# Optimization experiments

Measured on AMD Instinct MI355X. Metric: run time of the kernel, lower is better.

Reference implementation:

```python
import jax, jax.numpy as jnp
import numpy as np

KH = KW = 3
K = KH * KW
OG = 1  # offset_groups
WG = 1  # weight_groups
DIL = 1

def _conv_same(x, w):
    # stride-1 SAME NCHW conv, matching the keras offset/mask convs
    return jax.lax.conv_general_dilated(
        x, w, window_strides=(1, 1), padding='SAME',
        dimension_numbers=('NCHW', 'OIHW', 'NCHW'))

def _deform_conv2d(x, w, offset, mask):
    # x: [B,C,H,W]; w: [F, C//WG, KH, KW]
    # offset: [B, OG*2*K, H, W] laid out as (og, k, {dy,dx});
    # mask:   [B, OG*K, H, W]
    B, C, H, W = x.shape
    F = w.shape[0]
    pad_h = ((KH - 1) * DIL) // 2
    pad_w = ((KW - 1) * DIL) // 2
    ky = jnp.arange(KH) * DIL - pad_h
    kx = jnp.arange(KW) * DIL - pad_w
    kyy, kxx = jnp.meshgrid(ky, kx, indexing='ij')
    kyy = kyy.reshape(K).astype(x.dtype)
    kxx = kxx.reshape(K).astype(x.dtype)

    off = offset.reshape(B, OG, K, 2, H, W)
    dy = off[:, :, :, 0]  # [B,OG,K,H,W]
    dx = off[:, :, :, 1]
    oy = jnp.arange(H, dtype=x.dtype)
    ox = jnp.arange(W, dtype=x.dtype)
    y = oy[None, None, None, :, None] + kyy[None, None, :, None, None] + dy
    xq = ox[None, None, None, None, :] + kxx[None, None, :, None, None] + dx

    y0 = jnp.floor(y)
    x0 = jnp.floor(xq)
    wy = y - y0   # [B,OG,K,H,W]
    wx = xq - x0
    y0i = y0.astype(jnp.int32)
    x0i = x0.astype(jnp.int32)

    Cg = C // OG
    xg = x.reshape(B, OG, Cg, H * W)

    def gather(yi, xi):
        valid = (yi >= 0) & (yi < H) & (xi >= 0) & (xi < W)
        idx = jnp.clip(yi, 0, H - 1) * W + jnp.clip(xi, 0, W - 1)
        flat = idx.reshape(B, OG, 1, K * H * W)
        v = jnp.take_along_axis(xg, flat, axis=3)   # [B,OG,Cg,K*H*W]
        v = v.reshape(B, OG, Cg, K, H, W)
        return v * valid[:, :, None].astype(x.dtype)

    v00 = gather(y0i, x0i)
    v01 = gather(y0i, x0i + 1)
    v10 = gather(y0i + 1, x0i)
    v11 = gather(y0i + 1, x0i + 1)
    wy_ = wy[:, :, None]
    wx_ = wx[:, :, None]
    samp = (v00 * (1 - wy_) * (1 - wx_) + v01 * (1 - wy_) * wx_
            + v10 * wy_ * (1 - wx_) + v11 * wy_ * wx_)  # [B,OG,Cg,K,H,W]
    m = mask.reshape(B, OG, K, H, W)[:, :, None]
    samp = samp * m
    wr = w.reshape(F, OG, Cg, K)
    return jnp.einsum('bgckhw,fgck->bfhw', samp, wr)


def setup_inputs() -> dict:
    key = jax.random.key(0)
    k1, k2, k3, k4 = jax.random.split(key, 4)
    B, C, H, W = 8, 256, 64, 64
    F = 256
    x = jax.random.normal(k1, (B, C, H, W), dtype=jnp.float32)
    w_offset = jax.random.normal(k2, (OG * 2 * K, C, KH, KW), dtype=jnp.float32) * 0.01
    w_mask = jax.random.normal(k3, (OG * K, C, KH, KW), dtype=jnp.float32) * 0.01
    w_deform = jax.random.normal(k4, (F, C // WG, KH, KW), dtype=jnp.float32) * 0.05
    return {'x': x, 'w_offset': w_offset, 'w_mask': w_mask, 'w_deform': w_deform}


def reference(x, w_offset, w_mask, w_deform):
    offset = _conv_same(x, w_offset)                 # [B, 2K, H, W]
    mask = jax.nn.sigmoid(_conv_same(x, w_mask))     # [B, K, H, W]
    return _deform_conv2d(x, w_deform, offset, mask)
```

## Files before the change

### kernel.cpp

```cpp
#include <hip/hip_runtime.h>
#include <hip/hip_bf16.h>
#include <hip/hip_fp16.h>
#include <math.h>

constexpr int Bn = 8, Cn = 256, Hn = 64, Wn = 64, Fn = 256, Kn = 9;
constexpr int HWn = Hn * Wn;
constexpr int NM = Bn * Kn * HWn;
constexpr int NCH = 4;

using frag_ab = __attribute__((ext_vector_type(8))) short;
using frag_h  = __attribute__((ext_vector_type(8))) _Float16;
using f32x4   = __attribute__((ext_vector_type(4))) float;

__device__ inline ushort f2bf(float f) {
    union { float f; uint32_t u; } un{f};
    return (ushort)((un.u + 0x7FFF + ((un.u >> 16) & 1)) >> 16);
}
__device__ inline ushort f2h(float f) {
    __half h = __float2half_rn(f);
    return *reinterpret_cast<ushort*>(&h);
}

__global__ __launch_bounds__(256) void wtrans2(const float* __restrict__ wd,
                                               ushort* __restrict__ wB) {
    int i = blockIdx.x * 256 + threadIdx.x;
    if (i >= Fn * Cn * Kn) return;
    int ci = i & 7, fi = (i >> 3) & 15, G = (i >> 7) & 31, ft = (i >> 12) & 15, k = i >> 16;
    int f = ft * 16 + fi, c = G * 8 + ci;
    wB[i] = f2h(wd[(f * Cn + c) * 9 + k]);
}

__global__ __launch_bounds__(256) void wpack27(const float* __restrict__ wo,
                                               const float* __restrict__ wm,
                                               ushort* __restrict__ wA) {
    int i = blockIdx.x * 256 + threadIdx.x;
    if (i >= 73728) return;
    int ci = i & 7, l = (i >> 3) & 63, mt = (i >> 9) & 1, cblk = (i >> 10) & 7, tap = i >> 13;
    int m = mt * 16 + (l & 15);
    int c = cblk * 32 + ((l >> 4) & 3) * 8 + ci;
    float v = 0.f;
    if (m < 18)      v = wo[(m * Cn + c) * 9 + tap];
    else if (m < 27) v = wm[((m - 18) * Cn + c) * 9 + tap];
    wA[i] = f2bf(v);
}

__global__ __launch_bounds__(256) void xpose(const float* __restrict__ x,
                                             __half2* __restrict__ xh) {
    int i = blockIdx.x * 256 + threadIdx.x;
    int p = i & 4095, q = (i >> 12) & 3, b = i >> 14;
    const float* xp = x + (size_t)b * Cn * HWn + p;
    __half2* op = xh + (((size_t)b * 4096 + p) << 7) + q * 32;
#pragma unroll
    for (int j = 0; j < 32; ++j) {
        int c = q * 64 + 2 * j;
        op[j] = __float22half2_rn(make_float2(xp[(size_t)c * HWn],
                                              xp[(size_t)(c + 1) * HWn]));
    }
}

__global__ __launch_bounds__(256) void offconv27(const float* __restrict__ x,
                                                 const ushort* __restrict__ wA,
                                                 float* __restrict__ part) {
    __shared__ ushort xs[4][66][40];
    const int t = threadIdx.x;
    const int l = t & 63, w = t >> 6;
    const int li = l & 15, lg = l >> 4;
    const int rb = blockIdx.x, ch = blockIdx.y, b = blockIdx.z;
    const int h0 = rb * 2;
    const int rw = w >> 1, pt0 = (w & 1) * 2;

    f32x4 acc[2][2];
#pragma unroll
    for (int mt = 0; mt < 2; ++mt)
#pragma unroll
        for (int q = 0; q < 2; ++q) acc[mt][q] = (f32x4)0.f;

    const float* xb = x + (size_t)b * Cn * HWn;

#pragma unroll 1
    for (int cc = 0; cc < 2; ++cc) {
        const int cbase = ch * 64 + cc * 32;
        __syncthreads();
        for (int j = t; j < 1056; j += 256) {
            int cq = j / 264;
            int rem = j - cq * 264;
            int r = rem / 66, col = rem - r * 66;
            int rg = h0 - 1 + r, cg = col - 1;
            ushort u[8];
            if ((unsigned)rg < (unsigned)Hn && (unsigned)cg < (unsigned)Wn) {
                const float* xp = xb + (size_t)(cbase + cq * 8) * HWn + (rg << 6) + cg;
#pragma unroll
                for (int jj = 0; jj < 8; ++jj) u[jj] = f2bf(xp[(size_t)jj * HWn]);
            } else {
#pragma unroll
                for (int jj = 0; jj < 8; ++jj) u[jj] = 0;
            }
            *(int4*)&xs[r][col][cq * 8] =
                make_int4(u[0] | (u[1] << 16), u[2] | (u[3] << 16),
                          u[4] | (u[5] << 16), u[6] | (u[7] << 16));
        }
        __syncthreads();
        const int cblk = ch * 2 + cc;
#pragma unroll
        for (int tap = 0; tap < 9; ++tap) {
            const int ky = tap / 3, kx = tap - 3 * (tap / 3);
            frag_ab a0 = *(const frag_ab*)(wA + (size_t)((tap * 8 + cblk) * 2) * 512 + l * 8);
            frag_ab a1 = *(const frag_ab*)(wA + (size_t)((tap * 8 + cblk) * 2 + 1) * 512 + l * 8);
#pragma unroll
            for (int q = 0; q < 2; ++q) {
                frag_ab bf = *(const frag_ab*)&xs[rw + ky][(pt0 + q) * 16 + li + kx][lg * 8];
                acc[0][q] = __builtin_amdgcn_mfma_f32_16x16x32_bf16(a0, bf, acc[0][q], 0, 0, 0);
                acc[1][q] = __builtin_amdgcn_mfma_f32_16x16x32_bf16(a1, bf, acc[1][q], 0, 0, 0);
            }
        }
    }

    const int h = h0 + rw;
#pragma unroll
    for (int mt = 0; mt < 2; ++mt)
#pragma unroll
        for (int j = 0; j < 4; ++j) {
            int m = mt * 16 + lg * 4 + j;
            if (m < 27) {
#pragma unroll
                for (int q = 0; q < 2; ++q) {
                    int pixel = (pt0 + q) * 16 + li;
                    part[((size_t)((ch * Bn + b) * 27 + m) << 12) + (h << 6) + pixel] =
                        acc[mt][q][j];
                }
            }
        }
}

__global__ __launch_bounds__(256) void metafin9(const float* __restrict__ part,
                                                int4* __restrict__ mpack) {
    const int k = blockIdx.y;
    const int idx = blockIdx.x * 256 + threadIdx.x;
    const int b = idx >> 12, p = idx & 4095;
    const int h = p >> 6, w = p & 63;

    float dy = 0.f, dx = 0.f, ms = 0.f;
#pragma unroll
    for (int ch = 0; ch < NCH; ++ch) {
        size_t base = ((size_t)((ch * Bn + b) * 27) << 12) + p;
        dy += part[base + ((size_t)(2 * k) << 12)];
        dx += part[base + ((size_t)(2 * k + 1) << 12)];
        ms += part[base + ((size_t)(18 + k) << 12)];
    }
    float m = 1.f / (1.f + expf(-ms));
    float yy = (float)(h + k / 3 - 1) + dy;
    float xx = (float)(w + k % 3 - 1) + dx;
    float y0f = floorf(yy), x0f = floorf(xx);
    float wy = yy - y0f, wx = xx - x0f;
    int y0 = (int)y0f, x0 = (int)x0f;
    int y1 = y0 + 1, x1 = x0 + 1;
    bool vy0 = (unsigned)y0 < (unsigned)Hn;
    bool vx0 = (unsigned)x0 < (unsigned)Wn;
    bool vy1 = (unsigned)y1 < (unsigned)Hn;
    bool vx1 = (unsigned)x1 < (unsigned)Wn;
    int cy0 = min(max(y0, 0), Hn - 1), cx0 = min(max(x0, 0), Wn - 1);
    int cy1 = min(max(y1, 0), Hn - 1), cx1 = min(max(x1, 0), Wn - 1);
    float w00 = (vy0 && vx0) ? (1.f - wy) * (1.f - wx) * m : 0.f;
    float w01 = (vy0 && vx1) ? (1.f - wy) * wx * m : 0.f;
    float w10 = (vy1 && vx0) ? wy * (1.f - wx) * m : 0.f;
    float w11 = (vy1 && vx1) ? wy * wx * m : 0.f;
    int i00 = (cy0 << 6) + cx0, i01 = (cy0 << 6) + cx1;
    int i10 = (cy1 << 6) + cx0, i11 = (cy1 << 6) + cx1;
    union { struct { __half a, bh; } h; int i; } pz, pw;
    pz.h.a = __float2half_rn(w00); pz.h.bh = __float2half_rn(w01);
    pw.h.a = __float2half_rn(w10); pw.h.bh = __float2half_rn(w11);
    int q = ((b * 9 + k) << 12) + p;
    mpack[q] = make_int4(i00 | (i01 << 16), i10 | (i11 << 16), pz.i, pw.i);
}

__global__ __launch_bounds__(512, 4) void dconv(const uint32_t* __restrict__ xh,
                                                const ushort* __restrict__ wB,
                                                const int4* __restrict__ mpack,
                                                float* __restrict__ out) {
    __shared__ ushort sl[2][64][64];
    __shared__ int4 ml[9][64];
    const int t = threadIdx.x;
    const int l = t & 63, w = t >> 6;
    const int li = l & 15, lg = l >> 4;
    const int pu = (w << 3) + (l >> 3);
    const int g  = l & 7;
    const int b = blockIdx.x;
    const int p0 = blockIdx.y << 6;

    f32x4 acc[2][4];
#pragma unroll
    for (int a = 0; a < 2; ++a)
#pragma unroll
        for (int q = 0; q < 4; ++q) acc[a][q] = (f32x4)0.f;

    const uint32_t* xb = xh + ((size_t)b << 19);

    for (int j = t; j < 576; j += 512)
        ml[j >> 6][j & 63] = mpack[((b * 9 + (j >> 6)) << 12) + p0 + (j & 63)];
    __syncthreads();

    auto STAGE = [&](int s, int buf) {
        const int k = s % 9, ch = s / 9;
        const int4 m = ml[k][pu];
        const int i00 = m.x & 0xFFFF, i01 = ((unsigned)m.x) >> 16;
        const int i10 = m.y & 0xFFFF, i11 = ((unsigned)m.y) >> 16;
        union { int i; __half2 h; } uz, uw;
        uz.i = m.z; uw.i = m.w;
        const uint32_t* base = xb + (ch << 5) + (g << 2);
        uint4 v00 = *(const uint4*)(base + (size_t)i00 * 128);
        uint4 v01 = *(const uint4*)(base + (size_t)i01 * 128);
        uint4 v10 = *(const uint4*)(base + (size_t)i10 * 128);
        uint4 v11 = *(const uint4*)(base + (size_t)i11 * 128);
        const __half2 w00 = __half2half2(__low2half(uz.h));
        const __half2 w01 = __half2half2(__high2half(uz.h));
        const __half2 w10 = __half2half2(__low2half(uw.h));
        const __half2 w11 = __half2half2(__high2half(uw.h));
        uint4 rr;
        {
            __half2 r = __hmul2(w00, *(__half2*)&v00.x);
            r = __hfma2(w01, *(__half2*)&v01.x, r);
            r = __hfma2(w10, *(__half2*)&v10.x, r);
            r = __hfma2(w11, *(__half2*)&v11.x, r);
            rr.x = *(uint32_t*)&r;
        }
        {
            __half2 r = __hmul2(w00, *(__half2*)&v00.y);
            r = __hfma2(w01, *(__half2*)&v01.y, r);
            r = __hfma2(w10, *(__half2*)&v10.y, r);
            r = __hfma2(w11, *(__half2*)&v11.y, r);
            rr.y = *(uint32_t*)&r;
        }
        {
            __half2 r = __hmul2(w00, *(__half2*)&v00.z);
            r = __hfma2(w01, *(__half2*)&v01.z, r);
            r = __hfma2(w10, *(__half2*)&v10.z, r);
            r = __hfma2(w11, *(__half2*)&v11.z, r);
            rr.z = *(uint32_t*)&r;
        }
        {
            __half2 r = __hmul2(w00, *(__half2*)&v00.w);
            r = __hfma2(w01, *(__half2*)&v01.w, r);
            r = __hfma2(w10, *(__half2*)&v10.w, r);
            r = __hfma2(w11, *(__half2*)&v11.w, r);
            rr.w = *(uint32_t*)&r;
        }
        *(uint4*)&sl[buf][pu][(g ^ (pu & 7)) << 3] = rr;
    };

    auto COMPUTE = [&](int s, int buf) {
        const int k = s % 9, ch = s / 9;
        const ushort* wp = wB + ((size_t)((k * 16 + 2 * w) * 512 + ch * 128)) * 8;
#pragma unroll
        for (int h = 0; h < 2; ++h) {
            frag_h bq[4];
#pragma unroll
            for (int pt = 0; pt < 4; ++pt)
                bq[pt] = *(const frag_h*)&sl[buf][pt * 16 + li]
                                           [((((h << 2) | lg) ^ (l & 7)) << 3)];
#pragma unroll
            for (int ft = 0; ft < 2; ++ft) {
                frag_h a = *(const frag_h*)(wp + (size_t)(ft * 512 + h * 64 + l) * 8);
#pragma unroll
                for (int pt = 0; pt < 4; ++pt)
                    acc[ft][pt] = __builtin_amdgcn_mfma_f32_16x16x32_f16(
                        a, bq[pt], acc[ft][pt], 0, 0, 0);
            }
        }
    };

    STAGE(0, 0);
    __syncthreads();
#pragma unroll 1
    for (int s = 0; s < 36; ++s) {
        const int cur = s & 1;
        if (s + 1 < 36) STAGE(s + 1, cur ^ 1);
        COMPUTE(s, cur);
        __syncthreads();
    }

    float* ob = out + (size_t)b * Fn * HWn + p0;
#pragma unroll
    for (int ft = 0; ft < 2; ++ft)
#pragma unroll
        for (int j = 0; j < 4; ++j) {
            int f = w * 32 + ft * 16 + lg * 4 + j;
#pragma unroll
            for (int pt = 0; pt < 4; ++pt)
                ob[(size_t)f * HWn + pt * 16 + li] = acc[ft][pt][j];
        }
}

extern "C" void kernel_launch(void* const* d_in, const int* in_sizes, int n_in,
                              void* d_out, int out_size, void* d_ws, size_t ws_size,
                              hipStream_t stream) {
    const float* x  = (const float*)d_in[0];
    const float* wo = (const float*)d_in[1];
    const float* wm = (const float*)d_in[2];
    const float* wd = (const float*)d_in[3];
    float* out = (float*)d_out;

    int4*     mpack = (int4*)d_ws;
    char*     region = (char*)d_ws + (size_t)NM * 16;
    float*    part  = (float*)region;
    ushort*   wBp   = (ushort*)region;
    __half2*  xhh   = (__half2*)(region + 1179648);
    uint32_t* xhu   = (uint32_t*)(region + 1179648);
    ushort*   wA27  = (ushort*)(region + 18874368);

    wpack27<<<dim3(288), dim3(256), 0, stream>>>(wo, wm, wA27);
    offconv27<<<dim3(32, NCH, Bn), dim3(256), 0, stream>>>(x, wA27, part);
    metafin9<<<dim3(Bn * HWn / 256, 9), dim3(256), 0, stream>>>(part, mpack);
    wtrans2<<<dim3((Fn * Cn * Kn + 255) / 256), dim3(256), 0, stream>>>(wd, wBp);
    xpose<<<dim3(Bn * 4 * HWn / 256), dim3(256), 0, stream>>>(x, xhh);
    dconv<<<dim3(Bn, HWn / 64), dim3(512), 0, stream>>>(xhu, wBp, mpack, out);
}
```

Measured before the change: 106.1 us.

## Split gather into register prefetch and finish stages for deeper pipelining

Splits the bilinear gather stage into a global-load step that fills registers and a finish step that blends and writes to LDS. Loads for step s+2 are issued before the MFMA compute of step s, so gather latency is hidden across two compute phases instead of one. The main loop is unrolled by two with alternating register sets. This costs extra VGPRs for two in-flight sets of 4 uint4 loads, which may reduce occupancy.

```diff
diff --git a/kernel.cpp b/kernel.cpp
--- a/kernel.cpp
+++ b/kernel.cpp
@@ -199,49 +199,56 @@
         ml[j >> 6][j & 63] = mpack[((b * 9 + (j >> 6)) << 12) + p0 + (j & 63)];
     __syncthreads();
 
-    auto STAGE = [&](int s, int buf) {
+    struct GR { uint4 c00, c01, c10, c11; int wz, ww; };
+    GR gA, gB;
+
+    auto LOADG = [&](int s, GR& gr) {
         const int k = s % 9, ch = s / 9;
         const int4 m = ml[k][pu];
         const int i00 = m.x & 0xFFFF, i01 = ((unsigned)m.x) >> 16;
         const int i10 = m.y & 0xFFFF, i11 = ((unsigned)m.y) >> 16;
+        const uint32_t* base = xb + (ch << 5) + (g << 2);
+        gr.c00 = *(const uint4*)(base + (size_t)i00 * 128);
+        gr.c01 = *(const uint4*)(base + (size_t)i01 * 128);
+        gr.c10 = *(const uint4*)(base + (size_t)i10 * 128);
+        gr.c11 = *(const uint4*)(base + (size_t)i11 * 128);
+        gr.wz = m.z; gr.ww = m.w;
+    };
+
+    auto FINISH = [&](const GR& gr, int buf) {
         union { int i; __half2 h; } uz, uw;
-        uz.i = m.z; uw.i = m.w;
-        const uint32_t* base = xb + (ch << 5) + (g << 2);
-        uint4 v00 = *(const uint4*)(base + (size_t)i00 * 128);
-        uint4 v01 = *(const uint4*)(base + (size_t)i01 * 128);
-        uint4 v10 = *(const uint4*)(base + (size_t)i10 * 128);
-        uint4 v11 = *(const uint4*)(base + (size_t)i11 * 128);
+        uz.i = gr.wz; uw.i = gr.ww;
         const __half2 w00 = __half2half2(__low2half(uz.h));
         const __half2 w01 = __half2half2(__high2half(uz.h));
         const __half2 w10 = __half2half2(__low2half(uw.h));
         const __half2 w11 = __half2half2(__high2half(uw.h));
         uint4 rr;
         {
-            __half2 r = __hmul2(w00, *(__half2*)&v00.x);
-            r = __hfma2(w01, *(__half2*)&v01.x, r);
-            r = __hfma2(w10, *(__half2*)&v10.x, r);
-            r = __hfma2(w11, *(__half2*)&v11.x, r);
+            __half2 r = __hmul2(w00, *(const __half2*)&gr.c00.x);
+            r = __hfma2(w01, *(const __half2*)&gr.c01.x, r);
+            r = __hfma2(w10, *(const __half2*)&gr.c10.x, r);
+            r = __hfma2(w11, *(const __half2*)&gr.c11.x, r);
             rr.x = *(uint32_t*)&r;
         }
         {
-            __half2 r = __hmul2(w00, *(__half2*)&v00.y);
-            r = __hfma2(w01, *(__half2*)&v01.y, r);
-            r = __hfma2(w10, *(__half2*)&v10.y, r);
-            r = __hfma2(w11, *(__half2*)&v11.y, r);
+            __half2 r = __hmul2(w00, *(const __half2*)&gr.c00.y);
+            r = __hfma2(w01, *(const __half2*)&gr.c01.y, r);
+            r = __hfma2(w10, *(const __half2*)&gr.c10.y, r);
+            r = __hfma2(w11, *(const __half2*)&gr.c11.y, r);
             rr.y = *(uint32_t*)&r;
         }
         {
-            __half2 r = __hmul2(w00, *(__half2*)&v00.z);
-            r = __hfma2(w01, *(__half2*)&v01.z, r);
-            r = __hfma2(w10, *(__half2*)&v10.z, r);
-            r = __hfma2(w11, *(__half2*)&v11.z, r);
+            __half2 r = __hmul2(w00, *(const __half2*)&gr.c00.z);
+            r = __hfma2(w01, *(const __half2*)&gr.c01.z, r);
+            r = __hfma2(w10, *(const __half2*)&gr.c10.z, r);
+            r = __hfma2(w11, *(const __half2*)&gr.c11.z, r);
             rr.z = *(uint32_t*)&r;
         }
         {
-            __half2 r = __hmul2(w00, *(__half2*)&v00.w);
-            r = __hfma2(w01, *(__half2*)&v01.w, r);
-            r = __hfma2(w10, *(__half2*)&v10.w, r);
-            r = __hfma2(w11, *(__half2*)&v11.w, r);
+            __half2 r = __hmul2(w00, *(const __half2*)&gr.c00.w);
+            r = __hfma2(w01, *(const __half2*)&gr.c01.w, r);
+            r = __hfma2(w10, *(const __half2*)&gr.c10.w, r);
+            r = __hfma2(w11, *(const __half2*)&gr.c11.w, r);
             rr.w = *(uint32_t*)&r;
         }
         *(uint4*)&sl[buf][pu][(g ^ (pu & 7)) << 3] = rr;
@@ -268,13 +275,19 @@
         }
     };
 
-    STAGE(0, 0);
+    LOADG(0, gA);
+    LOADG(1, gB);
+    FINISH(gA, 0);
     __syncthreads();
 #pragma unroll 1
-    for (int s = 0; s < 36; ++s) {
-        const int cur = s & 1;
-        if (s + 1 < 36) STAGE(s + 1, cur ^ 1);
-        COMPUTE(s, cur);
+    for (int s = 0; s < 36; s += 2) {
+        if (s + 2 < 36) LOADG(s + 2, gA);
+        COMPUTE(s, 0);
+        FINISH(gB, 1);
+        __syncthreads();
+        if (s + 3 < 36) LOADG(s + 3, gB);
+        COMPUTE(s + 1, 1);
+        if (s + 2 < 36) FINISH(gA, 0);
         __syncthreads();
     }
 
```

New measurement: 112.0 us. +5.6%, slower.

## Split dconv into 1024-thread blocks with alternating stager groups and halved MFMA tiles

Applied to the files above, without the earlier changes.

Doubles the dconv workgroup to 16 waves. Each wave now computes 32 filters by 32 pixels instead of 32 by 64, which halves the accumulator registers per wave. The gather/bilinear staging work alternates between two groups of 8 waves on even and odd stages, so each wave stages only every other step. The goal is more waves in flight to hide gather latency and less register pressure. The cost is twice as many threads meeting at each barrier, and the same weight fragments are now loaded by two waves.

```diff
diff --git a/kernel.cpp b/kernel.cpp
--- a/kernel.cpp
+++ b/kernel.cpp
@@ -173,30 +173,34 @@
     mpack[q] = make_int4(i00 | (i01 << 16), i10 | (i11 << 16), pz.i, pw.i);
 }
 
-__global__ __launch_bounds__(512, 4) void dconv(const uint32_t* __restrict__ xh,
-                                                const ushort* __restrict__ wB,
-                                                const int4* __restrict__ mpack,
-                                                float* __restrict__ out) {
+__global__ __launch_bounds__(1024, 8) void dconv(const uint32_t* __restrict__ xh,
+                                                 const ushort* __restrict__ wB,
+                                                 const int4* __restrict__ mpack,
+                                                 float* __restrict__ out) {
     __shared__ ushort sl[2][64][64];
     __shared__ int4 ml[9][64];
     const int t = threadIdx.x;
     const int l = t & 63, w = t >> 6;
     const int li = l & 15, lg = l >> 4;
-    const int pu = (w << 3) + (l >> 3);
+    const int group = w >> 3;
+    const int sw = w & 7;
+    const int pu = (sw << 3) + (l >> 3);
     const int g  = l & 7;
+    const int fblk = w >> 1;
+    const int ph = w & 1;
     const int b = blockIdx.x;
     const int p0 = blockIdx.y << 6;
 
-    f32x4 acc[2][4];
+    f32x4 acc[2][2];
 #pragma unroll
     for (int a = 0; a < 2; ++a)
 #pragma unroll
-        for (int q = 0; q < 4; ++q) acc[a][q] = (f32x4)0.f;
+        for (int q = 0; q < 2; ++q) acc[a][q] = (f32x4)0.f;
 
     const uint32_t* xb = xh + ((size_t)b << 19);
 
-    for (int j = t; j < 576; j += 512)
-        ml[j >> 6][j & 63] = mpack[((b * 9 + (j >> 6)) << 12) + p0 + (j & 63)];
+    if (t < 576)
+        ml[t >> 6][t & 63] = mpack[((b * 9 + (t >> 6)) << 12) + p0 + (t & 63)];
     __syncthreads();
 
     auto STAGE = [&](int s, int buf) {
@@ -249,32 +253,31 @@
 
     auto COMPUTE = [&](int s, int buf) {
         const int k = s % 9, ch = s / 9;
-        const ushort* wp = wB + ((size_t)((k * 16 + 2 * w) * 512 + ch * 128)) * 8;
+        const ushort* wp = wB + ((size_t)((k * 16 + fblk * 2) * 512 + ch * 128)) * 8;
 #pragma unroll
         for (int h = 0; h < 2; ++h) {
-            frag_h bq[4];
-#pragma unroll
-            for (int pt = 0; pt < 4; ++pt)
-                bq[pt] = *(const frag_h*)&sl[buf][pt * 16 + li]
-                                           [((((h << 2) | lg) ^ (l & 7)) << 3)];
+            frag_h bq[2];
+#pragma unroll
+            for (int q = 0; q < 2; ++q)
+                bq[q] = *(const frag_h*)&sl[buf][(ph * 2 + q) * 16 + li]
+                                          [((((h << 2) | lg) ^ (l & 7)) << 3)];
 #pragma unroll
             for (int ft = 0; ft < 2; ++ft) {
                 frag_h a = *(const frag_h*)(wp + (size_t)(ft * 512 + h * 64 + l) * 8);
 #pragma unroll
-                for (int pt = 0; pt < 4; ++pt)
-                    acc[ft][pt] = __builtin_amdgcn_mfma_f32_16x16x32_f16(
-                        a, bq[pt], acc[ft][pt], 0, 0, 0);
+                for (int q = 0; q < 2; ++q)
+                    acc[ft][q] = __builtin_amdgcn_mfma_f32_16x16x32_f16(
+                        a, bq[q], acc[ft][q], 0, 0, 0);
             }
         }
     };
 
-    STAGE(0, 0);
+    if (group == 0) STAGE(0, 0);
     __syncthreads();
 #pragma unroll 1
     for (int s = 0; s < 36; ++s) {
-        const int cur = s & 1;
-        if (s + 1 < 36) STAGE(s + 1, cur ^ 1);
-        COMPUTE(s, cur);
+        if (s + 1 < 36 && group == ((s + 1) & 1)) STAGE(s + 1, (s + 1) & 1);
+        COMPUTE(s, s & 1);
         __syncthreads();
     }
 
@@ -283,10 +286,10 @@
     for (int ft = 0; ft < 2; ++ft)
 #pragma unroll
         for (int j = 0; j < 4; ++j) {
-            int f = w * 32 + ft * 16 + lg * 4 + j;
-#pragma unroll
-            for (int pt = 0; pt < 4; ++pt)
-                ob[(size_t)f * HWn + pt * 16 + li] = acc[ft][pt][j];
+            int f = fblk * 32 + ft * 16 + lg * 4 + j;
+#pragma unroll
+            for (int q = 0; q < 2; ++q)
+                ob[(size_t)f * HWn + (ph * 2 + q) * 16 + li] = acc[ft][q][j];
         }
 }
 
@@ -312,5 +315,5 @@
     metafin9<<<dim3(Bn * HWn / 256, 9), dim3(256), 0, stream>>>(part, mpack);
     wtrans2<<<dim3((Fn * Cn * Kn + 255) / 256), dim3(256), 0, stream>>>(wd, wBp);
     xpose<<<dim3(Bn * 4 * HWn / 256), dim3(256), 0, stream>>>(x, xhh);
-    dconv<<<dim3(Bn, HWn / 64), dim3(512), 0, stream>>>(xhu, wBp, mpack, out);
-}
+    dconv<<<dim3(Bn, HWn / 64), dim3(1024), 0, stream>>>(xhu, wBp, mpack, out);
+}
```

After: 114.1 us. 7.6% more time.

## Merge weight/input pack kernels and stage two steps per sync in dconv

Applied to the files above, without the earlier changes.

Fuses the weight transpose and the input fp16 transpose into one launch, using a block-index split to drop one kernel launch. In the deformable conv main loop, the LDS buffer becomes 2x2 so that two pipeline steps are staged and computed between barriers, halving the number of __syncthreads. The larger shared buffer (32KB for sl) may reduce occupancy under the 4-blocks-per-CU launch bound, and it raises register pressure from gathering two stages at once.

```diff
diff --git a/kernel.cpp b/kernel.cpp
--- a/kernel.cpp
+++ b/kernel.cpp
@@ -19,15 +19,6 @@
 __device__ inline ushort f2h(float f) {
     __half h = __float2half_rn(f);
     return *reinterpret_cast<ushort*>(&h);
-}
-
-__global__ __launch_bounds__(256) void wtrans2(const float* __restrict__ wd,
-                                               ushort* __restrict__ wB) {
-    int i = blockIdx.x * 256 + threadIdx.x;
-    if (i >= Fn * Cn * Kn) return;
-    int ci = i & 7, fi = (i >> 3) & 15, G = (i >> 7) & 31, ft = (i >> 12) & 15, k = i >> 16;
-    int f = ft * 16 + fi, c = G * 8 + ci;
-    wB[i] = f2h(wd[(f * Cn + c) * 9 + k]);
 }
 
 __global__ __launch_bounds__(256) void wpack27(const float* __restrict__ wo,
@@ -42,20 +33,6 @@
     if (m < 18)      v = wo[(m * Cn + c) * 9 + tap];
     else if (m < 27) v = wm[((m - 18) * Cn + c) * 9 + tap];
     wA[i] = f2bf(v);
-}
-
-__global__ __launch_bounds__(256) void xpose(const float* __restrict__ x,
-                                             __half2* __restrict__ xh) {
-    int i = blockIdx.x * 256 + threadIdx.x;
-    int p = i & 4095, q = (i >> 12) & 3, b = i >> 14;
-    const float* xp = x + (size_t)b * Cn * HWn + p;
-    __half2* op = xh + (((size_t)b * 4096 + p) << 7) + q * 32;
-#pragma unroll
-    for (int j = 0; j < 32; ++j) {
-        int c = q * 64 + 2 * j;
-        op[j] = __float22half2_rn(make_float2(xp[(size_t)c * HWn],
-                                              xp[(size_t)(c + 1) * HWn]));
-    }
 }
 
 __global__ __launch_bounds__(256) void offconv27(const float* __restrict__ x,
@@ -173,11 +150,35 @@
     mpack[q] = make_int4(i00 | (i01 << 16), i10 | (i11 << 16), pz.i, pw.i);
 }
 
+__global__ __launch_bounds__(256) void packBX(const float* __restrict__ wd,
+                                              const float* __restrict__ x,
+                                              ushort* __restrict__ wB,
+                                              __half2* __restrict__ xh) {
+    const int bid = blockIdx.x, t = threadIdx.x;
+    if (bid < 2304) {
+        int i = bid * 256 + t;
+        int ci = i & 7, fi = (i >> 3) & 15, G = (i >> 7) & 31, ft = (i >> 12) & 15, k = i >> 16;
+        int f = ft * 16 + fi, c = G * 8 + ci;
+        wB[i] = f2h(wd[(f * Cn + c) * 9 + k]);
+    } else {
+        int i = (bid - 2304) * 256 + t;
+        int p = i & 4095, q = (i >> 12) & 3, b = i >> 14;
+        const float* xp = x + (size_t)b * Cn * HWn + p;
+        __half2* op = xh + (((size_t)b * 4096 + p) << 7) + q * 32;
+#pragma unroll
+        for (int j = 0; j < 32; ++j) {
+            int c = q * 64 + 2 * j;
+            op[j] = __float22half2_rn(make_float2(xp[(size_t)c * HWn],
+                                                  xp[(size_t)(c + 1) * HWn]));
+        }
+    }
+}
+
 __global__ __launch_bounds__(512, 4) void dconv(const uint32_t* __restrict__ xh,
                                                 const ushort* __restrict__ wB,
                                                 const int4* __restrict__ mpack,
                                                 float* __restrict__ out) {
-    __shared__ ushort sl[2][64][64];
+    __shared__ ushort sl[2][2][64][64];
     __shared__ int4 ml[9][64];
     const int t = threadIdx.x;
     const int l = t & 63, w = t >> 6;
@@ -199,7 +200,7 @@
         ml[j >> 6][j & 63] = mpack[((b * 9 + (j >> 6)) << 12) + p0 + (j & 63)];
     __syncthreads();
 
-    auto STAGE = [&](int s, int buf) {
+    auto STAGE = [&](int s) {
         const int k = s % 9, ch = s / 9;
         const int4 m = ml[k][pu];
         const int i00 = m.x & 0xFFFF, i01 = ((unsigned)m.x) >> 16;
@@ -244,10 +245,10 @@
             r = __hfma2(w11, *(__half2*)&v11.w, r);
             rr.w = *(uint32_t*)&r;
         }
-        *(uint4*)&sl[buf][pu][(g ^ (pu & 7)) << 3] = rr;
+        *(uint4*)&sl[(s >> 1) & 1][s & 1][pu][(g ^ (pu & 7)) << 3] = rr;
     };
 
-    auto COMPUTE = [&](int s, int buf) {
+    auto COMPUTE = [&](int s) {
         const int k = s % 9, ch = s / 9;
         const ushort* wp = wB + ((size_t)((k * 16 + 2 * w) * 512 + ch * 128)) * 8;
 #pragma unroll
@@ -255,7 +256,7 @@
             frag_h bq[4];
 #pragma unroll
             for (int pt = 0; pt < 4; ++pt)
-                bq[pt] = *(const frag_h*)&sl[buf][pt * 16 + li]
+                bq[pt] = *(const frag_h*)&sl[(s >> 1) & 1][s & 1][pt * 16 + li]
                                            [((((h << 2) | lg) ^ (l & 7)) << 3)];
 #pragma unroll
             for (int ft = 0; ft < 2; ++ft) {
@@ -268,13 +269,17 @@
         }
     };
 
-    STAGE(0, 0);
+    STAGE(0);
+    STAGE(1);
     __syncthreads();
 #pragma unroll 1
-    for (int s = 0; s < 36; ++s) {
-        const int cur = s & 1;
-        if (s + 1 < 36) STAGE(s + 1, cur ^ 1);
-        COMPUTE(s, cur);
+    for (int s = 0; s < 36; s += 2) {
+        if (s + 2 < 36) {
+            STAGE(s + 2);
+            STAGE(s + 3);
+        }
+        COMPUTE(s);
+        COMPUTE(s + 1);
         __syncthreads();
     }
 
@@ -310,7 +315,6 @@
     wpack27<<<dim3(288), dim3(256), 0, stream>>>(wo, wm, wA27);
     offconv27<<<dim3(32, NCH, Bn), dim3(256), 0, stream>>>(x, wA27, part);
     metafin9<<<dim3(Bn * HWn / 256, 9), dim3(256), 0, stream>>>(part, mpack);
-    wtrans2<<<dim3((Fn * Cn * Kn + 255) / 256), dim3(256), 0, stream>>>(wd, wBp);
-    xpose<<<dim3(Bn * 4 * HWn / 256), dim3(256), 0, stream>>>(x, xhh);
+    packBX<<<dim3(2816), dim3(256), 0, stream>>>(wd, x, wBp, xhh);
     dconv<<<dim3(Bn, HWn / 64), dim3(512), 0, stream>>>(xhu, wBp, mpack, out);
 }
```

New measurement: 105.7 us. Within noise of the previous version (-0.4%).
